# Optimization experiments

Measured on AMD Instinct MI355X. Metric: run time of the kernel, lower is better.

Reference implementation:

```python
import jax, jax.numpy as jnp
import numpy as np

B, N, F_IN, F_OUT = 4, 2048, 128, 128

def setup_inputs() -> dict:
    key = jax.random.key(0)
    k1, k2, k3, k4 = jax.random.split(key, 4)
    node_features = jax.random.uniform(k1, (B, N, F_IN), dtype=jnp.float32)
    adjacency = jax.random.uniform(k2, (B, N, N), dtype=jnp.float32)
    # nn.Linear(in_dim, out_dim) params
    lim = 1.0 / np.sqrt(F_IN)
    W = jax.random.uniform(k3, (F_OUT, F_IN), minval=-lim, maxval=lim, dtype=jnp.float32)
    b = jax.random.uniform(k4, (F_OUT,), minval=-lim, maxval=lim, dtype=jnp.float32)
    return {"node_features": node_features, "adjacency": adjacency, "W": W, "b": b}

def reference(node_features, adjacency, W, b):
    # degree_inv_sqrt, same math as diag_embed matmuls but via row/col scaling
    degree = adjacency.sum(axis=-1)                              # [B, N]
    d_inv_sqrt = jnp.clip(degree, 1e-6, None) ** -0.5            # [B, N]
    norm_adj = adjacency * d_inv_sqrt[:, :, None] * d_inv_sqrt[:, None, :]  # [B, N, N]
    agg = jnp.einsum('bnm,bmf->bnf', norm_adj, node_features)    # [B, N, F_in]
    return agg @ W.T + b                                         # [B, N, F_out]
```

## Files before the change

kernel.cpp:

```cpp
#include <hip/hip_runtime.h>


#define NN 2048
#define FF 128
#define WS_NEED (32768u + 4u * 128u * 2048u * 2u)

typedef __attribute__((ext_vector_type(4))) float f32x4;
typedef __attribute__((ext_vector_type(8))) short short8;

__device__ inline unsigned short f2bf(float f) {
    unsigned u = __builtin_bit_cast(unsigned, f);
    u = (u + 0x7fffu + ((u >> 16) & 1u)) >> 16;
    return (unsigned short)u;
}

__device__ inline short8 cvt8(f32x4 a, f32x4 b) {
    short8 r;
    r[0] = (short)f2bf(a.x); r[1] = (short)f2bf(a.y);
    r[2] = (short)f2bf(a.z); r[3] = (short)f2bf(a.w);
    r[4] = (short)f2bf(b.x); r[5] = (short)f2bf(b.y);
    r[6] = (short)f2bf(b.z); r[7] = (short)f2bf(b.w);
    return r;
}

#define SOFT_BARRIER()                                           \
    do {                                                         \
        asm volatile("s_waitcnt lgkmcnt(0)" ::: "memory");       \
        __builtin_amdgcn_s_barrier();                            \
        asm volatile("" ::: "memory");                           \
    } while (0)

__global__ __launch_bounds__(256) void k1_deg(const float* __restrict__ A,
                                              float* __restrict__ dinv) {
    __shared__ float red[256];
    int row = blockIdx.x;
    int t = threadIdx.x;
    const f32x4* ap = (const f32x4*)(A + (size_t)row * NN);
    f32x4 v0 = ap[t];
    f32x4 v1 = ap[t + 256];
    red[t] = v0.x + v0.y + v0.z + v0.w + v1.x + v1.y + v1.z + v1.w;
    __syncthreads();
    #pragma unroll
    for (int s = 128; s > 0; s >>= 1) {
        if (t < s) red[t] += red[t + s];
        __syncthreads();
    }
    if (t == 0) dinv[row] = rsqrtf(fmaxf(red[0], 1e-6f));
}

__global__ __launch_bounds__(256) void k2_zt(const float* __restrict__ X,
                                             const float* __restrict__ W,
                                             const float* __restrict__ dinv,
                                             unsigned short* __restrict__ Zt) {
    __shared__ float Ws[FF * FF];
    int blk = blockIdx.x;
    int b  = blk >> 6;
    int mc = (blk >> 3) & 7;
    int oc = blk & 7;
    int t  = threadIdx.x;
    int m  = mc * 256 + t;

    {
        f32x4* wd = (f32x4*)Ws;
        const f32x4* wsrc = (const f32x4*)W;
        #pragma unroll
        for (int j = 0; j < 16; ++j) wd[t + 256 * j] = wsrc[t + 256 * j];
    }
    __syncthreads();

    float acc[16];
    #pragma unroll
    for (int j = 0; j < 16; ++j) acc[j] = 0.f;

    const f32x4* xr = (const f32x4*)(X + ((size_t)b * NN + m) * FF);
    for (int f4 = 0; f4 < FF / 4; ++f4) {
        f32x4 xv = xr[f4];
        #pragma unroll
        for (int j = 0; j < 16; ++j) {
            f32x4 wv = *(const f32x4*)&Ws[(oc * 16 + j) * FF + f4 * 4];
            acc[j] += xv.x * wv.x + xv.y * wv.y + xv.z * wv.z + xv.w * wv.w;
        }
    }
    float dv = dinv[b * NN + m];
    #pragma unroll
    for (int j = 0; j < 16; ++j)
        Zt[((size_t)b * FF + oc * 16 + j) * NN + m] = f2bf(acc[j] * dv);
}

__global__ __launch_bounds__(256) void k3_mfma(const float* __restrict__ A,
                                               const unsigned short* __restrict__ Zt,
                                               const float* __restrict__ dinv,
                                               const float* __restrict__ bias,
                                               float* __restrict__ out) {
    __shared__ unsigned short As[2][16][72];
    __shared__ unsigned short Zs[2][128][72];
    int blk = blockIdx.x;
    int b   = blk >> 7;
    int n0  = (blk & 127) * 16;
    int t   = threadIdx.x;
    int w   = t >> 6, lane = t & 63;
    int l15 = lane & 15, kgrp = (lane >> 4) * 8;

    const float* Ab = A + (size_t)b * NN * NN;
    const unsigned short* Zb = Zt + (size_t)b * FF * NN;

    int ar = t >> 3;
    int ac = (t & 7) * 8;
    int zo = t >> 1;
    int zk = (t & 1) * 32;

    f32x4 acc[2];
    acc[0] = (f32x4){0.f, 0.f, 0.f, 0.f};
    acc[1] = (f32x4){0.f, 0.f, 0.f, 0.f};

    f32x4 pa0, pa1;  short8 pz0, pz1, pz2, pz3;
    f32x4 qa0, qa1;  short8 qz0, qz1, qz2, qz3;

    #define LOADT(A0, A1, Z0, Z1, Z2, Z3, k0)                                \
        do {                                                                 \
            if (t < 128) {                                                   \
                const float* asrc = Ab + (size_t)(n0 + ar) * NN + (k0) + ac; \
                A0 = *(const f32x4*)asrc;                                    \
                A1 = *(const f32x4*)(asrc + 4);                              \
            }                                                                \
            const unsigned short* zsrc = Zb + (size_t)zo * NN + (k0) + zk;   \
            Z0 = *(const short8*)(zsrc);                                     \
            Z1 = *(const short8*)(zsrc + 8);                                 \
            Z2 = *(const short8*)(zsrc + 16);                                \
            Z3 = *(const short8*)(zsrc + 24);                                \
        } while (0)

    #define WRITET(buf, A0, A1, Z0, Z1, Z2, Z3)                              \
        do {                                                                 \
            if (t < 128) *(short8*)&As[buf][ar][ac] = cvt8(A0, A1);          \
            *(short8*)&Zs[buf][zo][zk]      = Z0;                            \
            *(short8*)&Zs[buf][zo][zk + 8]  = Z1;                            \
            *(short8*)&Zs[buf][zo][zk + 16] = Z2;                            \
            *(short8*)&Zs[buf][zo][zk + 24] = Z3;                            \
        } while (0)

    #define MFMAS(cur)                                                       \
        do {                                                                 \
            _Pragma("unroll")                                                \
            for (int ks = 0; ks < 64; ks += 32) {                            \
                short8 af = *(const short8*)&As[cur][l15][ks + kgrp];        \
                short8 bf0 = *(const short8*)&Zs[cur][w * 32 + l15][ks + kgrp];       \
                short8 bf1 = *(const short8*)&Zs[cur][w * 32 + 16 + l15][ks + kgrp];  \
                acc[0] = __builtin_amdgcn_mfma_f32_16x16x32_bf16(af, bf0, acc[0], 0, 0, 0); \
                acc[1] = __builtin_amdgcn_mfma_f32_16x16x32_bf16(af, bf1, acc[1], 0, 0, 0); \
            }                                                                \
        } while (0)

    LOADT(pa0, pa1, pz0, pz1, pz2, pz3, 0);
    WRITET(0, pa0, pa1, pz0, pz1, pz2, pz3);
    LOADT(pa0, pa1, pz0, pz1, pz2, pz3, 64);
    SOFT_BARRIER();

    for (int it = 0; it < 32; it += 2) {
        if (it + 2 < 32) LOADT(qa0, qa1, qz0, qz1, qz2, qz3, (it + 2) * 64);
        MFMAS(0);
        if (it + 1 < 32) WRITET(1, pa0, pa1, pz0, pz1, pz2, pz3);
        SOFT_BARRIER();
        if (it + 1 < 32) {
            if (it + 3 < 32) LOADT(pa0, pa1, pz0, pz1, pz2, pz3, (it + 3) * 64);
            MFMAS(1);
            if (it + 2 < 32) WRITET(0, qa0, qa1, qz0, qz1, qz2, qz3);
            SOFT_BARRIER();
        }
    }

    int drow = (lane >> 4) * 4;
    #pragma unroll
    for (int tt = 0; tt < 2; ++tt) {
        int o = w * 32 + tt * 16 + l15;
        float bv = bias[o];
        #pragma unroll
        for (int r = 0; r < 4; ++r) {
            int n = n0 + drow + r;
            float dv = dinv[b * NN + n];
            out[((size_t)b * NN + n) * FF + o] = dv * acc[tt][r] + bv;
        }
    }
    #undef LOADT
    #undef WRITET
    #undef MFMAS
}

extern "C" void kernel_launch(void* const* d_in, const int* in_sizes, int n_in,
                              void* d_out, int out_size, void* d_ws, size_t ws_size,
                              hipStream_t stream) {
    const float *X = nullptr, *A = nullptr, *W = nullptr, *bias = nullptr;
    for (int i = 0; i < n_in; ++i) {
        switch (in_sizes[i]) {
            case 16777216: A    = (const float*)d_in[i]; break;
            case 1048576:  X    = (const float*)d_in[i]; break;
            case 16384:    W    = (const float*)d_in[i]; break;
            case 128:      bias = (const float*)d_in[i]; break;
            default: break;
        }
    }
    float* out = (float*)d_out;
    if (!X || !A || !W || !bias) return;
    if (out_size != 4 * NN * FF) return;
    if (ws_size < (size_t)WS_NEED) return;

    float* dinv        = (float*)d_ws;
    unsigned short* Zt = (unsigned short*)((char*)d_ws + 32768);

    k1_deg<<<4 * NN, 256, 0, stream>>>(A, dinv);
    k2_zt<<<256, 256, 0, stream>>>(X, W, dinv, Zt);
    k3_mfma<<<512, 256, 0, stream>>>(A, Zt, dinv, bias, out);
}
```

Before: 52.23 us.

## Split aggregation GEMM over K and output columns with separate reduce kernel

Result: slower. 58.64 us (+12.3%).

```diff
diff --git a/kernel.cpp b/kernel.cpp
--- a/kernel.cpp
+++ b/kernel.cpp
@@ -3,7 +3,9 @@
 
 #define NN 2048
 #define FF 128
-#define WS_NEED (32768u + 4u * 128u * 2048u * 2u)
+#define ZT_OFF   32768u
+#define P_OFF    (ZT_OFF + 4u * 128u * 2048u * 2u)
+#define WS_NEED  (P_OFF + 2u * 4u * 2048u * 128u * 4u)
 
 typedef __attribute__((ext_vector_type(4))) float f32x4;
 typedef __attribute__((ext_vector_type(8))) short short8;
@@ -87,22 +89,22 @@
         Zt[((size_t)b * FF + oc * 16 + j) * NN + m] = f2bf(acc[j] * dv);
 }
 
-__global__ __launch_bounds__(256) void k3_mfma(const float* __restrict__ A,
-                                               const unsigned short* __restrict__ Zt,
-                                               const float* __restrict__ dinv,
-                                               const float* __restrict__ bias,
-                                               float* __restrict__ out) {
+__global__ __launch_bounds__(128) void k3_split(const float* __restrict__ A,
+                                                const unsigned short* __restrict__ Zt,
+                                                float* __restrict__ P) {
     __shared__ unsigned short As[2][16][72];
-    __shared__ unsigned short Zs[2][128][72];
+    __shared__ unsigned short Zs[2][64][72];
     int blk = blockIdx.x;
-    int b   = blk >> 7;
-    int n0  = (blk & 127) * 16;
+    int kh  = blk & 1;
+    int o0  = ((blk >> 1) & 1) * 64;
+    int n0  = ((blk >> 2) & 127) * 16;
+    int b   = blk >> 9;
     int t   = threadIdx.x;
     int w   = t >> 6, lane = t & 63;
     int l15 = lane & 15, kgrp = (lane >> 4) * 8;
 
-    const float* Ab = A + (size_t)b * NN * NN;
-    const unsigned short* Zb = Zt + (size_t)b * FF * NN;
+    const float* Ab = A + (size_t)b * NN * NN + (size_t)kh * 1024;
+    const unsigned short* Zb = Zt + (size_t)b * FF * NN + (size_t)kh * 1024;
 
     int ar = t >> 3;
     int ac = (t & 7) * 8;
@@ -118,12 +120,10 @@
 
     #define LOADT(A0, A1, Z0, Z1, Z2, Z3, k0)                                \
         do {                                                                 \
-            if (t < 128) {                                                   \
-                const float* asrc = Ab + (size_t)(n0 + ar) * NN + (k0) + ac; \
-                A0 = *(const f32x4*)asrc;                                    \
-                A1 = *(const f32x4*)(asrc + 4);                              \
-            }                                                                \
-            const unsigned short* zsrc = Zb + (size_t)zo * NN + (k0) + zk;   \
+            const float* asrc = Ab + (size_t)(n0 + ar) * NN + (k0) + ac;     \
+            A0 = *(const f32x4*)asrc;                                        \
+            A1 = *(const f32x4*)(asrc + 4);                                  \
+            const unsigned short* zsrc = Zb + (size_t)(o0 + zo) * NN + (k0) + zk; \
             Z0 = *(const short8*)(zsrc);                                     \
             Z1 = *(const short8*)(zsrc + 8);                                 \
             Z2 = *(const short8*)(zsrc + 16);                                \
@@ -132,7 +132,7 @@
 
     #define WRITET(buf, A0, A1, Z0, Z1, Z2, Z3)                              \
         do {                                                                 \
-            if (t < 128) *(short8*)&As[buf][ar][ac] = cvt8(A0, A1);          \
+            *(short8*)&As[buf][ar][ac] = cvt8(A0, A1);                       \
             *(short8*)&Zs[buf][zo][zk]      = Z0;                            \
             *(short8*)&Zs[buf][zo][zk + 8]  = Z1;                            \
             *(short8*)&Zs[buf][zo][zk + 16] = Z2;                            \
@@ -156,34 +156,54 @@
     LOADT(pa0, pa1, pz0, pz1, pz2, pz3, 64);
     SOFT_BARRIER();
 
-    for (int it = 0; it < 32; it += 2) {
-        if (it + 2 < 32) LOADT(qa0, qa1, qz0, qz1, qz2, qz3, (it + 2) * 64);
+    for (int it = 0; it < 16; it += 2) {
+        if (it + 2 < 16) LOADT(qa0, qa1, qz0, qz1, qz2, qz3, (it + 2) * 64);
         MFMAS(0);
-        if (it + 1 < 32) WRITET(1, pa0, pa1, pz0, pz1, pz2, pz3);
+        if (it + 1 < 16) WRITET(1, pa0, pa1, pz0, pz1, pz2, pz3);
         SOFT_BARRIER();
-        if (it + 1 < 32) {
-            if (it + 3 < 32) LOADT(pa0, pa1, pz0, pz1, pz2, pz3, (it + 3) * 64);
+        if (it + 1 < 16) {
+            if (it + 3 < 16) LOADT(pa0, pa1, pz0, pz1, pz2, pz3, (it + 3) * 64);
             MFMAS(1);
-            if (it + 2 < 32) WRITET(0, qa0, qa1, qz0, qz1, qz2, qz3);
+            if (it + 2 < 16) WRITET(0, qa0, qa1, qz0, qz1, qz2, qz3);
             SOFT_BARRIER();
         }
     }
 
+    float* Pk = P + (size_t)kh * (4u * NN * FF);
     int drow = (lane >> 4) * 4;
     #pragma unroll
     for (int tt = 0; tt < 2; ++tt) {
-        int o = w * 32 + tt * 16 + l15;
-        float bv = bias[o];
+        int o = o0 + w * 32 + tt * 16 + l15;
         #pragma unroll
         for (int r = 0; r < 4; ++r) {
             int n = n0 + drow + r;
-            float dv = dinv[b * NN + n];
-            out[((size_t)b * NN + n) * FF + o] = dv * acc[tt][r] + bv;
+            Pk[((size_t)b * NN + n) * FF + o] = acc[tt][r];
         }
     }
     #undef LOADT
     #undef WRITET
     #undef MFMAS
+}
+
+__global__ __launch_bounds__(256) void k3_reduce(const float* __restrict__ P,
+                                                 const float* __restrict__ dinv,
+                                                 const float* __restrict__ bias,
+                                                 float* __restrict__ out) {
+    int idx = blockIdx.x * 256 + threadIdx.x;
+    int row = idx >> 5;
+    int c4  = idx & 31;
+    const f32x4* P0 = (const f32x4*)P;
+    const f32x4* P1 = P0 + (size_t)4 * NN * FF / 4;
+    f32x4 p = P0[idx];
+    f32x4 q = P1[idx];
+    f32x4 bv = ((const f32x4*)bias)[c4];
+    float dv = dinv[row];
+    f32x4 r;
+    r.x = (p.x + q.x) * dv + bv.x;
+    r.y = (p.y + q.y) * dv + bv.y;
+    r.z = (p.z + q.z) * dv + bv.z;
+    r.w = (p.w + q.w) * dv + bv.w;
+    ((f32x4*)out)[idx] = r;
 }
 
 extern "C" void kernel_launch(void* const* d_in, const int* in_sizes, int n_in,
@@ -205,9 +225,11 @@
     if (ws_size < (size_t)WS_NEED) return;
 
     float* dinv        = (float*)d_ws;
-    unsigned short* Zt = (unsigned short*)((char*)d_ws + 32768);
+    unsigned short* Zt = (unsigned short*)((char*)d_ws + ZT_OFF);
+    float* P           = (float*)((char*)d_ws + P_OFF);
 
     k1_deg<<<4 * NN, 256, 0, stream>>>(A, dinv);
     k2_zt<<<256, 256, 0, stream>>>(X, W, dinv, Zt);
-    k3_mfma<<<512, 256, 0, stream>>>(A, Zt, dinv, bias, out);
-}
+    k3_split<<<2048, 128, 0, stream>>>(A, Zt, P);
+    k3_reduce<<<1024, 256, 0, stream>>>(P, dinv, bias, out);
+}
```
